# Kernel tuning notes

Measured on AMD Instinct MI355X. Metric: run time of the kernel, lower is better.

Reference implementation:

```python
import jax, jax.numpy as jnp
import numpy as np

B, T, LQ, LC = 8, 256, 20, 10
DIM, H = 128, 8
VDIM, WDIM, CDIM = 1024, 300, 50
WORDS, CHARS = 10000, 100


def _build_edges(T, B):
    """Replicates build_graph_edges(hops=2) + build_semantic_edges + build_query_edges,
    then expand_edge_index_for_batch with num_nodes = T + 1.  Static numpy (jit-safe)."""
    N = T + 1
    es = []
    for h in (1, 2):  # temporal edges, 2 hops (indices replicate original code exactly)
        i = np.arange(T - h)
        es += [np.stack([i, i + h]), np.stack([i + h, i])]
    i = np.arange(T)  # query<->segment edges inside build_graph_edges
    z = np.zeros(T, dtype=np.int64)
    es += [np.stack([z, i + 1]), np.stack([i + 1, z])]
    temporal = np.concatenate(es, axis=1)
    a, b = np.triu_indices(T, k=1)  # torch.combinations(arange(T), r=2)
    sem = np.concatenate([np.stack([a, b]), np.stack([b, a])], axis=1)
    qe = np.stack([np.concatenate([[0], np.arange(1, T + 1)]),
                   np.concatenate([np.arange(1, T + 1), [0]])])
    off = (np.arange(B, dtype=np.int64) * N)[None, :, None]
    expand = lambda e: (e[:, None, :].astype(np.int64) + off).reshape(2, -1)
    return np.concatenate([expand(temporal), expand(sem), expand(qe)], axis=1)


def setup_inputs() -> dict:
    key = jax.random.key(0)
    ks = jax.random.split(key, 16)
    w = lambda k, shape: jax.random.normal(k, shape, jnp.float32) * 0.02
    return {
        "word_ids": jax.random.randint(ks[0], (B, LQ), 0, WORDS),
        "char_ids": jax.random.randint(ks[1], (B, LQ, LC), 0, CHARS),
        "video_features": jax.random.normal(ks[2], (B, T, VDIM), jnp.float32),
        "v_mask": jnp.ones((B, T), jnp.float32),
        "q_mask": jnp.ones((B, LQ), jnp.float32),
        "word_emb": w(ks[3], (WORDS, WDIM)),
        "char_emb": w(ks[4], (CHARS, CDIM)),
        "W_embed": w(ks[5], (WDIM + CDIM, DIM)), "b_embed": jnp.zeros((DIM,), jnp.float32),
        "W_vproj": w(ks[6], (VDIM, DIM)), "b_vproj": jnp.zeros((DIM,), jnp.float32),
        "W_enc": w(ks[7], (DIM, DIM)), "b_enc": jnp.zeros((DIM,), jnp.float32),
        "Wq": w(ks[8], (DIM, DIM)), "bq": jnp.zeros((DIM,), jnp.float32),
        "Wk": w(ks[9], (DIM, DIM)), "bk": jnp.zeros((DIM,), jnp.float32),
        "Wv": w(ks[10], (DIM, DIM)), "bv": jnp.zeros((DIM,), jnp.float32),
        "Wskip": w(ks[11], (DIM, DIM)), "bskip": jnp.zeros((DIM,), jnp.float32),
        "W_start": w(ks[12], (DIM, 1)), "b_start": jnp.zeros((1,), jnp.float32),
        "W_end": w(ks[13], (DIM, 1)), "b_end": jnp.zeros((1,), jnp.float32),
    }


def reference(word_ids, char_ids, video_features, v_mask, q_mask,
              word_emb, char_emb, W_embed, b_embed, W_vproj, b_vproj,
              W_enc, b_enc, Wq, bq, Wk, bk, Wv, bv, Wskip, bskip,
              W_start, b_start, W_end, b_end):
    enc = lambda x, m: jax.nn.relu(x @ W_enc + b_enc) * m[..., None]  # shared feature encoder (stand-in)
    # video branch
    vfeat = enc(video_features @ W_vproj + b_vproj, v_mask)            # [B, T, DIM]
    # query branch: word + char embeddings -> dim, encode, mean-pool
    qemb = jnp.concatenate([word_emb[word_ids], char_emb[char_ids].mean(axis=2)], axis=-1)
    qfeat = enc(qemb @ W_embed + b_embed, q_mask).mean(axis=1)         # [B, DIM]
    nodes = jnp.concatenate([qfeat[:, None, :], vfeat], axis=1)        # [B, N, DIM], N = T+1
    Bn, N, _ = nodes.shape
    Nn = Bn * N
    xf = nodes.reshape(Nn, DIM)
    edges = jnp.asarray(_build_edges(N - 1, Bn))                       # [2, E] static
    src, dst = edges[0], edges[1]                                      # PyG: messages x_j=src -> target i=dst
    hd = DIM // H
    q = (xf @ Wq + bq).reshape(Nn, H, hd)
    k = (xf @ Wk + bk).reshape(Nn, H, hd)
    v = (xf @ Wv + bv).reshape(Nn, H, hd)
    # TransformerConv: per-edge attention logits, segment-softmax over incoming edges
    logits = (q[dst] * k[src]).sum(-1) / float(np.sqrt(hd))            # [E, H]
    mx = jax.ops.segment_max(logits, dst, num_segments=Nn)
    ex = jnp.exp(logits - mx[dst])
    den = jax.ops.segment_sum(ex, dst, num_segments=Nn)
    alpha = ex / (den[dst] + 1e-16)
    agg = jax.ops.segment_sum(alpha[:, :, None] * v[src], dst, num_segments=Nn)  # [Nn, H, hd]
    out = agg.reshape(Nn, DIM) + xf @ Wskip + bskip                    # root_weight skip connection
    out = out.reshape(Bn, N, DIM)
    start_logits = (out[:, 1:] @ W_start + b_start)[..., 0]            # [B, T]
    end_logits = (out[:, 1:] @ W_end + b_end)[..., 0]                  # [B, T]
    return start_logits, end_logits
```

## Files before the change

### kernel.cpp

```cpp
#include <hip/hip_runtime.h>
#include <hip/hip_bf16.h>
#include <math.h>

#define B_ 8
#define T_ 256
#define LQ_ 20
#define LC_ 10
#define DIM_ 128
#define N_ 257
#define NN_ (B_*N_)

__global__ __launch_bounds__(256) void kNODE(
    const float* __restrict__ video, const float* __restrict__ Wv,
    const float* __restrict__ bvp,
    const float* __restrict__ We, const float* __restrict__ be,
    const float* __restrict__ vmask,
    const int* __restrict__ word_ids, const int* __restrict__ char_ids,
    const float* __restrict__ word_emb, const float* __restrict__ char_emb,
    const float* __restrict__ W_embed, const float* __restrict__ b_embed,
    const float* __restrict__ q_mask,
    const float* __restrict__ Wq, const float* __restrict__ bq,
    const float* __restrict__ Wk, const float* __restrict__ bk,
    const float* __restrict__ Wvv, const float* __restrict__ bval,
    const float* __restrict__ Ws, const float* __restrict__ bs,
    float* __restrict__ q, float* __restrict__ k,
    float* __restrict__ v, float* __restrict__ sk,
    float* __restrict__ eq)
{
  __shared__ float smem[8 * 1024];
  __shared__ float ps2[2][8][128];
  __shared__ float xe[8][132];
  const int blk = blockIdx.x, tid = threadIdx.x;
  const float* Wm[4] = {Wq, Wk, Wvv, Ws};
  const float* bm[4] = {bq, bk, bval, bs};
  float* om[4] = {q, k, v, sk};

  if (blk < 160) {
    const int qi = blk;
    const int b = qi / 20, lq = qi - b * 20;
    float* emb = smem;
    float* ps  = smem + 352;
    float* hl  = smem + 608;
    float* pe  = smem + 736;
    const int wid = word_ids[b * LQ_ + lq];
    for (int m = tid; m < 300; m += 256) emb[m] = word_emb[(size_t)wid * 300 + m];
    if (tid < 50) {
      float s = 0.f;
      #pragma unroll
      for (int l = 0; l < 10; ++l) {
        const int cid = char_ids[(b * LQ_ + lq) * 10 + l];
        s += char_emb[cid * 50 + tid];
      }
      emb[300 + tid] = s * 0.1f;
    }
    __syncthreads();
    const int j = tid & 127, half = tid >> 7;
    float a = 0.f;
    const float* Wcol = W_embed + (size_t)(half * 175) * 128 + j;
    const float* eh = emb + half * 175;
    #pragma unroll 5
    for (int m = 0; m < 175; ++m) a += eh[m] * Wcol[(size_t)m * 128];
    ps[half * 128 + j] = a;
    __syncthreads();
    if (tid < 128) hl[tid] = ps[tid] + ps[128 + tid] + b_embed[tid];
    __syncthreads();
    float e = 0.f;
    #pragma unroll 8
    for (int kk = 0; kk < 64; ++kk)
      e += hl[half * 64 + kk] * We[(half * 64 + kk) * 128 + j];
    pe[half * 128 + j] = e;
    __syncthreads();
    if (tid < 128) {
      float ev = pe[tid] + pe[128 + tid] + be[tid];
      ev = fmaxf(ev, 0.f) * q_mask[b * LQ_ + lq];
      eq[(size_t)qi * 128 + tid] = ev;
    }
  } else {
    const int r0 = (blk - 160) * 8;
    float (*Vl)[1024] = reinterpret_cast<float(*)[1024]>(smem);
    {
      const float4* src = reinterpret_cast<const float4*>(video + (size_t)r0 * 1024);
      float4* dst = reinterpret_cast<float4*>(smem);
      #pragma unroll
      for (int i = 0; i < 8; ++i) dst[tid + i * 256] = src[tid + i * 256];
    }
    __syncthreads();
    const int jc = tid & 31, rg = tid >> 5;
    {
      const int half = rg >> 2, rp = rg & 3;
      const int ra = rp * 2, rb = ra + 1;
      const float4* W4 = reinterpret_cast<const float4*>(Wv) + (size_t)half * 512 * 32 + jc;
      const float* va = &Vl[ra][half * 512];
      const float* vb = &Vl[rb][half * 512];
      float4 a0 = {0,0,0,0}, a1 = {0,0,0,0};
      #pragma unroll 8
      for (int kk = 0; kk < 512; ++kk) {
        const float4 w = W4[(size_t)kk * 32];
        const float x0 = va[kk], x1 = vb[kk];
        a0.x += x0*w.x; a0.y += x0*w.y; a0.z += x0*w.z; a0.w += x0*w.w;
        a1.x += x1*w.x; a1.y += x1*w.y; a1.z += x1*w.z; a1.w += x1*w.w;
      }
      *reinterpret_cast<float4*>(&ps2[half][ra][4 * jc]) = a0;
      *reinterpret_cast<float4*>(&ps2[half][rb][4 * jc]) = a1;
    }
    __syncthreads();
    float* hl = smem;
    {
      const float4 p0 = *reinterpret_cast<const float4*>(&ps2[0][rg][4 * jc]);
      const float4 p1 = *reinterpret_cast<const float4*>(&ps2[1][rg][4 * jc]);
      const float4 bb = reinterpret_cast<const float4*>(bvp)[jc];
      float4 hh;
      hh.x = p0.x + p1.x + bb.x; hh.y = p0.y + p1.y + bb.y;
      hh.z = p0.z + p1.z + bb.z; hh.w = p0.w + p1.w + bb.w;
      *reinterpret_cast<float4*>(&hl[rg * 128 + 4 * jc]) = hh;
    }
    __syncthreads();
    {
      const float4* We4 = reinterpret_cast<const float4*>(We) + jc;
      float4 a = reinterpret_cast<const float4*>(be)[jc];
      const float* hr = &hl[rg * 128];
      #pragma unroll 8
      for (int kk = 0; kk < 128; ++kk) {
        const float4 w = We4[kk * 32];
        const float x = hr[kk];
        a.x += x*w.x; a.y += x*w.y; a.z += x*w.z; a.w += x*w.w;
      }
      const float mk = vmask[r0 + rg];
      a.x = fmaxf(a.x, 0.f) * mk; a.y = fmaxf(a.y, 0.f) * mk;
      a.z = fmaxf(a.z, 0.f) * mk; a.w = fmaxf(a.w, 0.f) * mk;
      *reinterpret_cast<float4*>(&xe[rg][4 * jc]) = a;
    }
    __syncthreads();
    {
      const int m = rg & 3, g = rg >> 2;
      const float4* W4p = reinterpret_cast<const float4*>(Wm[m]) + jc;
      const float4 bb = reinterpret_cast<const float4*>(bm[m])[jc];
      float4 ac0 = bb, ac1 = bb, ac2 = bb, ac3 = bb;
      #pragma unroll 4
      for (int kk = 0; kk < 128; ++kk) {
        const float4 w = W4p[kk * 32];
        const float x0 = xe[4*g+0][kk], x1 = xe[4*g+1][kk];
        const float x2 = xe[4*g+2][kk], x3 = xe[4*g+3][kk];
        ac0.x += x0*w.x; ac0.y += x0*w.y; ac0.z += x0*w.z; ac0.w += x0*w.w;
        ac1.x += x1*w.x; ac1.y += x1*w.y; ac1.z += x1*w.z; ac1.w += x1*w.w;
        ac2.x += x2*w.x; ac2.y += x2*w.y; ac2.z += x2*w.z; ac2.w += x2*w.w;
        ac3.x += x3*w.x; ac3.y += x3*w.y; ac3.z += x3*w.z; ac3.w += x3*w.w;
      }
      float4 acs[4] = {ac0, ac1, ac2, ac3};
      #pragma unroll
      for (int r = 0; r < 4; ++r) {
        const int vr = r0 + 4 * g + r;
        const int node = (vr >> 8) * 257 + 1 + (vr & 255);
        *reinterpret_cast<float4*>(om[m] + (size_t)node * 128 + 4 * jc) = acs[r];
      }
    }
  }
}

__device__ __forceinline__ float cntf(int dnode, int s) {
  if (dnode == 256) return (s == 0 ? 1.f : 0.f) + (s == 255 ? 1.f : 0.f);
  float c = (s != dnode) ? 1.f : 0.f;
  if (s == 0) c += 1.f;
  if (s == dnode - 1) c += 2.f;
  if (s == dnode + 1 && dnode <= 254) c += 1.f;
  if (s == dnode - 2 && dnode >= 2) c += 1.f;
  if (s == dnode + 2 && dnode <= 253) c += 1.f;
  return c;
}

__global__ __launch_bounds__(256) void kATTN(
    const float* __restrict__ q, const float* __restrict__ k,
    const float* __restrict__ v, const float* __restrict__ eq,
    const float* __restrict__ Wk, const float* __restrict__ bk,
    const float* __restrict__ Wvv, const float* __restrict__ bval,
    float* __restrict__ npart, float* __restrict__ dpart)
{
  __shared__ float Kl[32][128];
  __shared__ float Vl[32][128];
  __shared__ float m0[128];
  const int d0 = blockIdx.x * 32;
  const int y  = blockIdx.y;
  const int b  = blockIdx.z;
  const int tid = threadIdx.x;
  const int base = b * 257;
  const int s0 = y * 32;
  {
    const float4* ksrc = reinterpret_cast<const float4*>(k + (size_t)(base + s0) * 128);
    const float4* vsrc = reinterpret_cast<const float4*>(v + (size_t)(base + s0) * 128);
    float4* kd = reinterpret_cast<float4*>(Kl);
    float4* vd = reinterpret_cast<float4*>(Vl);
    #pragma unroll
    for (int i = 0; i < 4; ++i) {
      kd[tid + i * 256] = ksrc[tid + i * 256];
      vd[tid + i * 256] = vsrc[tid + i * 256];
    }
  }
  if (y == 0 && tid < 128) {
    float s = 0.f;
    #pragma unroll 4
    for (int lq = 0; lq < LQ_; ++lq) s += eq[((size_t)b * LQ_ + lq) * 128 + tid];
    m0[tid] = s * (1.f / LQ_);
  }
  const int dd = tid >> 3, h = tid & 7;
  const int dnode = d0 + dd + 1;
  const float* qrow = q + (size_t)(base + dnode) * 128 + h * 16;
  const float4 qq0 = *(const float4*)(qrow + 0);
  const float4 qq1 = *(const float4*)(qrow + 4);
  const float4 qq2 = *(const float4*)(qrow + 8);
  const float4 qq3 = *(const float4*)(qrow + 12);
  __syncthreads();
  if (y == 0) {
    const int j = tid & 127, half = tid >> 7;
    const float* W = half ? Wvv : Wk;
    float acc = half ? bval[j] : bk[j];
    #pragma unroll 8
    for (int kk = 0; kk < 128; ++kk) acc += m0[kk] * W[kk * 128 + j];
    if (half) Vl[0][j] = acc; else Kl[0][j] = acc;
  }
  __syncthreads();

  float den = 0.f;
  float4 o0 = {0,0,0,0}, o1 = {0,0,0,0}, o2 = {0,0,0,0}, o3 = {0,0,0,0};
  #pragma unroll 2
  for (int s = 0; s < 32; ++s) {
    const float* krow = &Kl[s][h * 16];
    const float4 k0 = *(const float4*)(krow + 0);
    const float4 k1 = *(const float4*)(krow + 4);
    const float4 k2 = *(const float4*)(krow + 8);
    const float4 k3 = *(const float4*)(krow + 12);
    float dt = qq0.x*k0.x + qq0.y*k0.y + qq0.z*k0.z + qq0.w*k0.w
             + qq1.x*k1.x + qq1.y*k1.y + qq1.z*k1.z + qq1.w*k1.w
             + qq2.x*k2.x + qq2.y*k2.y + qq2.z*k2.z + qq2.w*k2.w
             + qq3.x*k3.x + qq3.y*k3.y + qq3.z*k3.z + qq3.w*k3.w;
    const float c = cntf(dnode, s0 + s);
    const float pw = c * __expf(dt * 0.25f);
    den += pw;
    const float* vrow = &Vl[s][h * 16];
    const float4 v0 = *(const float4*)(vrow + 0);
    const float4 v1 = *(const float4*)(vrow + 4);
    const float4 v2 = *(const float4*)(vrow + 8);
    const float4 v3 = *(const float4*)(vrow + 12);
    o0.x += pw*v0.x; o0.y += pw*v0.y; o0.z += pw*v0.z; o0.w += pw*v0.w;
    o1.x += pw*v1.x; o1.y += pw*v1.y; o1.z += pw*v1.z; o1.w += pw*v1.w;
    o2.x += pw*v2.x; o2.y += pw*v2.y; o2.z += pw*v2.z; o2.w += pw*v2.w;
    o3.x += pw*v3.x; o3.y += pw*v3.y; o3.z += pw*v3.z; o3.w += pw*v3.w;
  }
  const size_t pb = ((size_t)y * 8 + b) * 256 + d0;
  float* np = npart + (pb + dd) * 128 + h * 16;
  *reinterpret_cast<float4*>(np + 0)  = o0;
  *reinterpret_cast<float4*>(np + 4)  = o1;
  *reinterpret_cast<float4*>(np + 8)  = o2;
  *reinterpret_cast<float4*>(np + 12) = o3;
  dpart[(pb + dd) * 8 + h] = den;
}

__global__ __launch_bounds__(256) void k_red(
    const float* __restrict__ npart, const float* __restrict__ dpart,
    const float* __restrict__ sk,
    const float* __restrict__ W_start, const float* __restrict__ b_start,
    const float* __restrict__ W_end, const float* __restrict__ b_end,
    float* __restrict__ out)
{
  __shared__ float red[16][2][2];
  const int d0 = blockIdx.x * 16;
  const int b = blockIdx.y;
  const int tid = threadIdx.x;
  const int base = b * 257;
  const int jB = tid & 127, shB = tid >> 7;
  const int hB = jB >> 4;
  const float wst = W_start[jB], wen = W_end[jB];
  #pragma unroll
  for (int dd8 = 0; dd8 < 8; ++dd8) {
    const int dd = shB * 8 + dd8;
    const int dst = d0 + dd;
    float num = 0.f, den = 0.f;
    #pragma unroll
    for (int y = 0; y < 8; ++y) {
      const size_t pb = ((size_t)y * 8 + b) * 256 + dst;
      num += npart[pb * 128 + jB];
      den += dpart[pb * 8 + hB];
    }
    const float o = num / (den + 1e-16f) + sk[(size_t)(base + dst + 1) * 128 + jB];
    float psum = o * wst, pesum = o * wen;
    #pragma unroll
    for (int off = 1; off < 64; off <<= 1) {
      psum += __shfl_xor(psum, off);
      pesum += __shfl_xor(pesum, off);
    }
    if ((tid & 63) == 0) { red[dd][jB >> 6][0] = psum; red[dd][jB >> 6][1] = pesum; }
  }
  __syncthreads();
  if (tid < 16) {
    out[b * 256 + d0 + tid]        = red[tid][0][0] + red[tid][1][0] + b_start[0];
    out[2048 + b * 256 + d0 + tid] = red[tid][0][1] + red[tid][1][1] + b_end[0];
  }
}

extern "C" void kernel_launch(void* const* d_in, const int* in_sizes, int n_in,
                              void* d_out, int out_size, void* d_ws, size_t ws_size,
                              hipStream_t stream) {
  const int*   word_ids = (const int*)d_in[0];
  const int*   char_ids = (const int*)d_in[1];
  const float* video    = (const float*)d_in[2];
  const float* v_mask   = (const float*)d_in[3];
  const float* q_mask   = (const float*)d_in[4];
  const float* word_emb = (const float*)d_in[5];
  const float* char_emb = (const float*)d_in[6];
  const float* W_embed  = (const float*)d_in[7];
  const float* b_embed  = (const float*)d_in[8];
  const float* W_vproj  = (const float*)d_in[9];
  const float* b_vproj  = (const float*)d_in[10];
  const float* W_enc    = (const float*)d_in[11];
  const float* b_enc    = (const float*)d_in[12];
  const float* Wq       = (const float*)d_in[13];
  const float* bq       = (const float*)d_in[14];
  const float* Wk       = (const float*)d_in[15];
  const float* bk       = (const float*)d_in[16];
  const float* Wv       = (const float*)d_in[17];
  const float* bv       = (const float*)d_in[18];
  const float* Wskip    = (const float*)d_in[19];
  const float* bskip    = (const float*)d_in[20];
  const float* W_start  = (const float*)d_in[21];
  const float* b_start  = (const float*)d_in[22];
  const float* W_end    = (const float*)d_in[23];
  const float* b_end    = (const float*)d_in[24];

  float* q     = (float*)d_ws;
  float* k     = q  + NN_ * DIM_;
  float* v     = k  + NN_ * DIM_;
  float* sk    = v  + NN_ * DIM_;
  float* eq    = sk + NN_ * DIM_;
  float* npart = eq + 160 * 128;
  float* dpart = npart + (size_t)8 * 8 * 256 * 128;

  hipLaunchKernelGGL(kNODE, dim3(416), dim3(256), 0, stream,
    video, W_vproj, b_vproj, W_enc, b_enc, v_mask,
    word_ids, char_ids, word_emb, char_emb, W_embed, b_embed, q_mask,
    Wq, bq, Wk, bk, Wv, bv, Wskip, bskip, q, k, v, sk, eq);
  hipLaunchKernelGGL(kATTN, dim3(8, 8, 8), dim3(256), 0, stream,
    q, k, v, eq, Wk, bk, Wv, bv, npart, dpart);
  hipLaunchKernelGGL(k_red, dim3(16, 8), dim3(256), 0, stream,
    npart, dpart, sk, W_start, b_start, W_end, b_end, (float*)d_out);
}
```

Measured before the change: 68.67 us.

## Split video node kernel into column-split projection and per-matrix epilogue kernels

The fused node kernel, which ran on 416 blocks, is split in two. The first kernel splits the 1024-to-128 video projection by output column quarter and reduces across K slices in shared memory, using 1184 blocks. The second kernel recomputes the encoder layer per row tile and assigns one of the four Q/K/V/skip projections to each block, using 1024 blocks. The goal is to expose more parallelism across the GPU's compute units. In exchange it adds a kernel launch, a global round trip for the intermediate h, and encoder matmul work repeated four times.

Result: slower. 85.65 us (+24.7%).

```diff
diff --git a/kernel.cpp b/kernel.cpp
--- a/kernel.cpp
+++ b/kernel.cpp
@@ -10,38 +10,27 @@
 #define N_ 257
 #define NN_ (B_*N_)
 
-__global__ __launch_bounds__(256) void kNODE(
+__global__ __launch_bounds__(256) void kHQ(
     const float* __restrict__ video, const float* __restrict__ Wv,
     const float* __restrict__ bvp,
-    const float* __restrict__ We, const float* __restrict__ be,
-    const float* __restrict__ vmask,
     const int* __restrict__ word_ids, const int* __restrict__ char_ids,
     const float* __restrict__ word_emb, const float* __restrict__ char_emb,
     const float* __restrict__ W_embed, const float* __restrict__ b_embed,
+    const float* __restrict__ We, const float* __restrict__ be,
     const float* __restrict__ q_mask,
-    const float* __restrict__ Wq, const float* __restrict__ bq,
-    const float* __restrict__ Wk, const float* __restrict__ bk,
-    const float* __restrict__ Wvv, const float* __restrict__ bval,
-    const float* __restrict__ Ws, const float* __restrict__ bs,
-    float* __restrict__ q, float* __restrict__ k,
-    float* __restrict__ v, float* __restrict__ sk,
-    float* __restrict__ eq)
+    float* __restrict__ h, float* __restrict__ eq)
 {
-  __shared__ float smem[8 * 1024];
-  __shared__ float ps2[2][8][128];
-  __shared__ float xe[8][132];
+  __shared__ float Vl[8][1028];
+  __shared__ float4 ps4[8][8][8];
   const int blk = blockIdx.x, tid = threadIdx.x;
-  const float* Wm[4] = {Wq, Wk, Wvv, Ws};
-  const float* bm[4] = {bq, bk, bval, bs};
-  float* om[4] = {q, k, v, sk};
 
   if (blk < 160) {
     const int qi = blk;
     const int b = qi / 20, lq = qi - b * 20;
-    float* emb = smem;
-    float* ps  = smem + 352;
-    float* hl  = smem + 608;
-    float* pe  = smem + 736;
+    float* emb = &Vl[0][0];
+    float* ps  = emb + 352;
+    float* hl  = emb + 608;
+    float* pe  = emb + 736;
     const int wid = word_ids[b * LQ_ + lq];
     for (int m = tid; m < 300; m += 256) emb[m] = word_emb[(size_t)wid * 300 + m];
     if (tid < 50) {
@@ -76,84 +65,104 @@
       eq[(size_t)qi * 128 + tid] = ev;
     }
   } else {
-    const int r0 = (blk - 160) * 8;
-    float (*Vl)[1024] = reinterpret_cast<float(*)[1024]>(smem);
+    const int vb = blk - 160;
+    const int cq = vb >> 8, rt = vb & 255;
+    const int r0 = rt * 8;
     {
       const float4* src = reinterpret_cast<const float4*>(video + (size_t)r0 * 1024);
-      float4* dst = reinterpret_cast<float4*>(smem);
       #pragma unroll
-      for (int i = 0; i < 8; ++i) dst[tid + i * 256] = src[tid + i * 256];
-    }
-    __syncthreads();
-    const int jc = tid & 31, rg = tid >> 5;
-    {
-      const int half = rg >> 2, rp = rg & 3;
-      const int ra = rp * 2, rb = ra + 1;
-      const float4* W4 = reinterpret_cast<const float4*>(Wv) + (size_t)half * 512 * 32 + jc;
-      const float* va = &Vl[ra][half * 512];
-      const float* vb = &Vl[rb][half * 512];
-      float4 a0 = {0,0,0,0}, a1 = {0,0,0,0};
-      #pragma unroll 8
-      for (int kk = 0; kk < 512; ++kk) {
-        const float4 w = W4[(size_t)kk * 32];
-        const float x0 = va[kk], x1 = vb[kk];
-        a0.x += x0*w.x; a0.y += x0*w.y; a0.z += x0*w.z; a0.w += x0*w.w;
-        a1.x += x1*w.x; a1.y += x1*w.y; a1.z += x1*w.z; a1.w += x1*w.w;
+      for (int i = 0; i < 8; ++i) {
+        const int idx4 = tid + i * 256;
+        const int r = idx4 >> 8, f = idx4 & 255;
+        reinterpret_cast<float4*>(&Vl[r][0])[f] = src[r * 256 + f];
       }
-      *reinterpret_cast<float4*>(&ps2[half][ra][4 * jc]) = a0;
-      *reinterpret_cast<float4*>(&ps2[half][rb][4 * jc]) = a1;
-    }
-    __syncthreads();
-    float* hl = smem;
-    {
-      const float4 p0 = *reinterpret_cast<const float4*>(&ps2[0][rg][4 * jc]);
-      const float4 p1 = *reinterpret_cast<const float4*>(&ps2[1][rg][4 * jc]);
-      const float4 bb = reinterpret_cast<const float4*>(bvp)[jc];
-      float4 hh;
-      hh.x = p0.x + p1.x + bb.x; hh.y = p0.y + p1.y + bb.y;
-      hh.z = p0.z + p1.z + bb.z; hh.w = p0.w + p1.w + bb.w;
-      *reinterpret_cast<float4*>(&hl[rg * 128 + 4 * jc]) = hh;
-    }
-    __syncthreads();
-    {
-      const float4* We4 = reinterpret_cast<const float4*>(We) + jc;
-      float4 a = reinterpret_cast<const float4*>(be)[jc];
-      const float* hr = &hl[rg * 128];
-      #pragma unroll 8
-      for (int kk = 0; kk < 128; ++kk) {
-        const float4 w = We4[kk * 32];
-        const float x = hr[kk];
-        a.x += x*w.x; a.y += x*w.y; a.z += x*w.z; a.w += x*w.w;
+    }
+    __syncthreads();
+    const int jc = tid & 7, rg = tid >> 3;
+    const int ke = rg >> 2, rp = rg & 3;
+    const int ra = 2 * rp, rb = ra + 1;
+    const float4* W4 = reinterpret_cast<const float4*>(Wv) + cq * 8 + jc;
+    const float* va = &Vl[ra][ke * 128];
+    const float* vb_ = &Vl[rb][ke * 128];
+    float4 a0 = {0,0,0,0}, a1 = {0,0,0,0};
+    #pragma unroll 8
+    for (int kk = 0; kk < 128; ++kk) {
+      const float4 w = W4[(size_t)(ke * 128 + kk) * 32];
+      const float x0 = va[kk], x1 = vb_[kk];
+      a0.x += x0*w.x; a0.y += x0*w.y; a0.z += x0*w.z; a0.w += x0*w.w;
+      a1.x += x1*w.x; a1.y += x1*w.y; a1.z += x1*w.z; a1.w += x1*w.w;
+    }
+    ps4[ke][ra][jc] = a0;
+    ps4[ke][rb][jc] = a1;
+    __syncthreads();
+    if (tid < 64) {
+      const int row = tid >> 3, c4 = tid & 7;
+      float4 s = reinterpret_cast<const float4*>(bvp)[cq * 8 + c4];
+      #pragma unroll
+      for (int ke2 = 0; ke2 < 8; ++ke2) {
+        const float4 p = ps4[ke2][row][c4];
+        s.x += p.x; s.y += p.y; s.z += p.z; s.w += p.w;
       }
-      const float mk = vmask[r0 + rg];
-      a.x = fmaxf(a.x, 0.f) * mk; a.y = fmaxf(a.y, 0.f) * mk;
-      a.z = fmaxf(a.z, 0.f) * mk; a.w = fmaxf(a.w, 0.f) * mk;
-      *reinterpret_cast<float4*>(&xe[rg][4 * jc]) = a;
-    }
-    __syncthreads();
-    {
-      const int m = rg & 3, g = rg >> 2;
-      const float4* W4p = reinterpret_cast<const float4*>(Wm[m]) + jc;
-      const float4 bb = reinterpret_cast<const float4*>(bm[m])[jc];
-      float4 ac0 = bb, ac1 = bb, ac2 = bb, ac3 = bb;
-      #pragma unroll 4
-      for (int kk = 0; kk < 128; ++kk) {
-        const float4 w = W4p[kk * 32];
-        const float x0 = xe[4*g+0][kk], x1 = xe[4*g+1][kk];
-        const float x2 = xe[4*g+2][kk], x3 = xe[4*g+3][kk];
-        ac0.x += x0*w.x; ac0.y += x0*w.y; ac0.z += x0*w.z; ac0.w += x0*w.w;
-        ac1.x += x1*w.x; ac1.y += x1*w.y; ac1.z += x1*w.z; ac1.w += x1*w.w;
-        ac2.x += x2*w.x; ac2.y += x2*w.y; ac2.z += x2*w.z; ac2.w += x2*w.w;
-        ac3.x += x3*w.x; ac3.y += x3*w.y; ac3.z += x3*w.z; ac3.w += x3*w.w;
-      }
-      float4 acs[4] = {ac0, ac1, ac2, ac3};
-      #pragma unroll
-      for (int r = 0; r < 4; ++r) {
-        const int vr = r0 + 4 * g + r;
-        const int node = (vr >> 8) * 257 + 1 + (vr & 255);
-        *reinterpret_cast<float4*>(om[m] + (size_t)node * 128 + 4 * jc) = acs[r];
-      }
-    }
+      *reinterpret_cast<float4*>(h + (size_t)(r0 + row) * 128 + cq * 32 + c4 * 4) = s;
+    }
+  }
+}
+
+__global__ __launch_bounds__(256) void kEP(
+    const float* __restrict__ h,
+    const float* __restrict__ We, const float* __restrict__ be,
+    const float* __restrict__ vmask,
+    const float* __restrict__ Wq, const float* __restrict__ bq,
+    const float* __restrict__ Wk, const float* __restrict__ bk,
+    const float* __restrict__ Wvv, const float* __restrict__ bval,
+    const float* __restrict__ Ws, const float* __restrict__ bs,
+    float* __restrict__ q, float* __restrict__ k,
+    float* __restrict__ v, float* __restrict__ sk)
+{
+  __shared__ float hl[8][128];
+  __shared__ float xe[8][132];
+  const int blk = blockIdx.x, tid = threadIdx.x;
+  const int rt = blk >> 2, m = blk & 3;
+  const int r0 = rt * 8;
+  const float* Wm[4] = {Wq, Wk, Wvv, Ws};
+  const float* bm[4] = {bq, bk, bval, bs};
+  float* om[4] = {q, k, v, sk};
+  {
+    const int r = tid >> 5, c4 = tid & 31;
+    reinterpret_cast<float4*>(&hl[r][0])[c4] =
+      reinterpret_cast<const float4*>(h + (size_t)r0 * 128)[tid];
+  }
+  __syncthreads();
+  const int jc = tid & 31, rg = tid >> 5;
+  {
+    const float4* We4 = reinterpret_cast<const float4*>(We) + jc;
+    float4 a = reinterpret_cast<const float4*>(be)[jc];
+    const float* hr = &hl[rg][0];
+    #pragma unroll 8
+    for (int kk = 0; kk < 128; ++kk) {
+      const float4 w = We4[kk * 32];
+      const float x = hr[kk];
+      a.x += x*w.x; a.y += x*w.y; a.z += x*w.z; a.w += x*w.w;
+    }
+    const float mk = vmask[r0 + rg];
+    a.x = fmaxf(a.x, 0.f) * mk; a.y = fmaxf(a.y, 0.f) * mk;
+    a.z = fmaxf(a.z, 0.f) * mk; a.w = fmaxf(a.w, 0.f) * mk;
+    *reinterpret_cast<float4*>(&xe[rg][4 * jc]) = a;
+  }
+  __syncthreads();
+  {
+    const float4* W4p = reinterpret_cast<const float4*>(Wm[m]) + jc;
+    float4 ac = reinterpret_cast<const float4*>(bm[m])[jc];
+    const float* xr = &xe[rg][0];
+    #pragma unroll 8
+    for (int kk = 0; kk < 128; ++kk) {
+      const float4 w = W4p[kk * 32];
+      const float x = xr[kk];
+      ac.x += x*w.x; ac.y += x*w.y; ac.z += x*w.z; ac.w += x*w.w;
+    }
+    const int vr = r0 + rg;
+    const int node = (vr >> 8) * 257 + 1 + (vr & 255);
+    *reinterpret_cast<float4*>(om[m] + (size_t)node * 128 + 4 * jc) = ac;
   }
 }
 
@@ -254,7 +263,7 @@
   dpart[(pb + dd) * 8 + h] = den;
 }
 
-__global__ __launch_bounds__(256) void k_red(
+__global__ __launch_bounds__(256) void kRED(
     const float* __restrict__ npart, const float* __restrict__ dpart,
     const float* __restrict__ sk,
     const float* __restrict__ W_start, const float* __restrict__ b_start,
@@ -330,15 +339,18 @@
   float* v     = k  + NN_ * DIM_;
   float* sk    = v  + NN_ * DIM_;
   float* eq    = sk + NN_ * DIM_;
-  float* npart = eq + 160 * 128;
+  float* h     = eq + 160 * 128;
+  float* npart = h  + 2048 * 128;
   float* dpart = npart + (size_t)8 * 8 * 256 * 128;
 
-  hipLaunchKernelGGL(kNODE, dim3(416), dim3(256), 0, stream,
-    video, W_vproj, b_vproj, W_enc, b_enc, v_mask,
-    word_ids, char_ids, word_emb, char_emb, W_embed, b_embed, q_mask,
-    Wq, bq, Wk, bk, Wv, bv, Wskip, bskip, q, k, v, sk, eq);
+  hipLaunchKernelGGL(kHQ, dim3(1184), dim3(256), 0, stream,
+    video, W_vproj, b_vproj, word_ids, char_ids, word_emb, char_emb,
+    W_embed, b_embed, W_enc, b_enc, q_mask, h, eq);
+  hipLaunchKernelGGL(kEP, dim3(1024), dim3(256), 0, stream,
+    h, W_enc, b_enc, v_mask, Wq, bq, Wk, bk, Wv, bv, Wskip, bskip,
+    q, k, v, sk);
   hipLaunchKernelGGL(kATTN, dim3(8, 8, 8), dim3(256), 0, stream,
     q, k, v, eq, Wk, bk, Wv, bv, npart, dpart);
-  hipLaunchKernelGGL(k_red, dim3(16, 8), dim3(256), 0, stream,
+  hipLaunchKernelGGL(kRED, dim3(16, 8), dim3(256), 0, stream,
     npart, dpart, sk, W_start, b_start, W_end, b_end, (float*)d_out);
 }
```
